# Kernel tuning notes

Hardware: AMD Instinct MI355X
Metric: run time of the kernel (lower is better)

## Reference

```python
import jax, jax.numpy as jnp
import numpy as np

N_NODES = 100000
N_EDGES = 3200000
D_IN = 128
D_OUT = 128
BN_EPS = 1e-5


def setup_inputs() -> dict:
    key = jax.random.key(0)
    k1, k2, k3, k4, k5 = jax.random.split(key, 5)
    x = jax.random.normal(k1, (N_NODES, D_IN), dtype=jnp.float32)
    edge_index = jax.random.randint(k2, (2, N_EDGES), 0, N_NODES, dtype=jnp.int64)
    s = 1.0 / np.sqrt(D_IN)
    W_l = jax.random.uniform(k3, (D_IN, D_OUT), minval=-s, maxval=s, dtype=jnp.float32)
    b_l = jnp.zeros((D_OUT,), dtype=jnp.float32)
    W_r = jax.random.uniform(k4, (D_IN, D_OUT), minval=-s, maxval=s, dtype=jnp.float32)
    gamma = jnp.ones((D_OUT,), dtype=jnp.float32)
    beta = jnp.zeros((D_OUT,), dtype=jnp.float32)
    return {"x": x, "edge_index": edge_index, "W_l": W_l, "b_l": b_l,
            "W_r": W_r, "gamma": gamma, "beta": beta}


def _sage_bn(x, edge_index, W_l, b_l, W_r, gamma, beta):
    src, dst = edge_index[0], edge_index[1]
    # gather source features, scatter-sum at targets, divide by in-degree (mean aggr)
    agg_sum = jax.ops.segment_sum(x[src], dst, num_segments=N_NODES)  # [N, D_IN]
    deg = jax.ops.segment_sum(jnp.ones((N_EDGES,), x.dtype), dst, num_segments=N_NODES)
    agg = agg_sum / jnp.maximum(deg, 1.0)[:, None]
    # SAGEConv: lin_l(aggregated) + lin_r(self)
    x_raw = agg @ W_l + b_l + x @ W_r  # [N, D_OUT]
    # BatchNorm1d (training mode: batch stats, biased variance)
    mu = jnp.mean(x_raw, axis=0)
    var = jnp.var(x_raw, axis=0)
    x_deskewed = (x_raw - mu) * jax.lax.rsqrt(var + BN_EPS) * gamma + beta
    return x_raw, x_deskewed


def reference(x, edge_index, W_l, b_l, W_r, gamma, beta):
    return _sage_bn(x, edge_index, W_l, b_l, W_r, gamma, beta)
```

## Files before the change

kernel.cpp:

```cpp
#include <hip/hip_runtime.h>

constexpr int NN = 100000;
constexpr int NE = 3200000;
constexpr int DD = 128;
constexpr int NB = 782;
constexpr int RND = 8192;
#define BN_EPS 1e-5f

typedef __attribute__((ext_vector_type(8))) short bf16x8;
typedef __attribute__((ext_vector_type(4))) float f32x4;
typedef __attribute__((ext_vector_type(2))) float f32x2;

constexpr size_t WS_CNT   = 0;
constexpr size_t WS_COFF  = 4096;
constexpr size_t WS_CUR   = 8192;
constexpr size_t WS_FLAG  = 12288;
constexpr size_t WS_BNSUM = 12800;
constexpr size_t WS_BNSQ  = 13312;
constexpr size_t WS_ZERO  = 16384;
constexpr size_t WS_DEG   = 16384;
constexpr size_t WS_OFF   = 416384;
constexpr size_t WS_CSR   = 816384;
constexpr size_t WS_WT    = 13616384;

__device__ inline unsigned bf16rne(float f) {
    unsigned u = __float_as_uint(f);
    return (u + 0x7fffu + ((u >> 16) & 1u)) >> 16;
}

#if __has_builtin(__builtin_amdgcn_cvt_pk_f32_fp8)
__device__ inline f32x2 fp8pk_lo(unsigned u) {
    return __builtin_amdgcn_cvt_pk_f32_fp8((int)u, false);
}
__device__ inline f32x2 fp8pk_hi(unsigned u) {
    return __builtin_amdgcn_cvt_pk_f32_fp8((int)u, true);
}
__device__ inline unsigned f32x4_to_fp8(float4 v) {
    int w = __builtin_amdgcn_cvt_pk_fp8_f32(v.x, v.y, 0, false);
    w = __builtin_amdgcn_cvt_pk_fp8_f32(v.z, v.w, w, true);
    return (unsigned)w;
}
#else
__device__ inline float fp8_to_f32_1(unsigned b) {
    unsigned s = (b & 0x80u) << 24;
    unsigned em = b & 0x7fu;
    float f;
    if (em >= 8) f = __uint_as_float((em << 20) + (120u << 23));
    else f = (float)em * 0.001953125f;
    return __uint_as_float(__float_as_uint(f) | s);
}
__device__ inline f32x2 fp8pk_lo(unsigned u) {
    f32x2 r;
    r[0] = fp8_to_f32_1(u & 0xffu);
    r[1] = fp8_to_f32_1((u >> 8) & 0xffu);
    return r;
}
__device__ inline f32x2 fp8pk_hi(unsigned u) {
    f32x2 r;
    r[0] = fp8_to_f32_1((u >> 16) & 0xffu);
    r[1] = fp8_to_f32_1((u >> 24) & 0xffu);
    return r;
}
__device__ inline unsigned f32_to_fp8_1(float f) {
    unsigned s = (__float_as_uint(f) >> 24) & 0x80u;
    float a = fabsf(f);
    if (!(a > 0.f)) return s;
    if (a >= 448.f) return s | 0x7Eu;
    int e = (int)(__float_as_uint(a) >> 23) - 127;
    if (e < -6) e = -6;
    float step = __uint_as_float((unsigned)(e - 3 + 127) << 23);
    int m = (int)rintf(a / step);
    if (m >= 16) { e += 1; m = 8; }
    if (m >= 8) return s | (unsigned)((e + 7) << 3) | (unsigned)(m - 8);
    return s | (unsigned)m;
}
__device__ inline unsigned f32x4_to_fp8(float4 v) {
    return f32_to_fp8_1(v.x) | (f32_to_fp8_1(v.y) << 8) |
           (f32_to_fp8_1(v.z) << 16) | (f32_to_fp8_1(v.w) << 24);
}
#endif

#define ACC8(u)                                                              \
    {                                                                        \
        aa0 += fp8pk_lo((u).x);                                              \
        aa1 += fp8pk_hi((u).x);                                              \
        aa2 += fp8pk_lo((u).y);                                              \
        aa3 += fp8pk_hi((u).y);                                              \
    }

__global__ void k_detect(const int* __restrict__ ei, int* __restrict__ flag) {
    int lane = threadIdx.x;
    int v = ei[2 * lane + 1];
    unsigned long long b = __ballot(v == 0);
    if (lane == 0) *flag = (b == ~0ull) ? 1 : 0;
}

__global__ __launch_bounds__(256) void k_prep(const float* __restrict__ x,
                                              unsigned* __restrict__ xb,
                                              unsigned* __restrict__ xq,
                                              const float* __restrict__ Wl,
                                              const float* __restrict__ Wr,
                                              unsigned short* __restrict__ Wt) {
    int bid = blockIdx.x;
    if (bid < 2048) {
        int total = NN * DD / 4;
        for (int i = bid * 256 + threadIdx.x; i < total; i += 2048 * 256) {
            float4 v = ((const float4*)x)[i];
            unsigned a = (bf16rne(v.y) << 16) | bf16rne(v.x);
            unsigned b = (bf16rne(v.w) << 16) | bf16rne(v.z);
            ((uint2*)xb)[i] = make_uint2(a, b);
            xq[i] = f32x4_to_fp8(v);
        }
    } else {
        int idx = (bid - 2048) * 256 + threadIdx.x;
        int n = idx >> 8, k = idx & 255;
        float v = (k < 128) ? Wl[(size_t)k * DD + n] : Wr[(size_t)(k - 128) * DD + n];
        Wt[idx] = (unsigned short)bf16rne(v);
    }
}

__global__ __launch_bounds__(256) void k_bcount(const int* __restrict__ ei,
                                                const int* __restrict__ flag,
                                                int* __restrict__ cnt) {
    __shared__ int hist[NB];
    for (int i = threadIdx.x; i < NB; i += 256) hist[i] = 0;
    __syncthreads();
    int i64 = *flag;
    int stride = gridDim.x * 256;
    for (int e = blockIdx.x * 256 + threadIdx.x; e < NE; e += stride) {
        int dst = i64 ? ei[2 * (NE + e)] : ei[NE + e];
        atomicAdd(&hist[dst >> 7], 1);
    }
    __syncthreads();
    for (int i = threadIdx.x; i < NB; i += 256) {
        int c = hist[i];
        if (c) atomicAdd(&cnt[i], c);
    }
}

__global__ __launch_bounds__(256) void k_scan(const int* __restrict__ cnt,
                                              int* __restrict__ coff,
                                              int* __restrict__ cur) {
    __shared__ int s[NB];
    for (int i = threadIdx.x; i < NB; i += 256) s[i] = cnt[i];
    __syncthreads();
    if (threadIdx.x == 0) {
        int acc = 0;
        for (int i = 0; i < NB; ++i) { int c = s[i]; s[i] = acc; acc += c; }
    }
    __syncthreads();
    for (int i = threadIdx.x; i < NB; i += 256) { coff[i] = s[i]; cur[i] = s[i]; }
    if (threadIdx.x == 0) coff[NB] = NE;
}

__global__ __launch_bounds__(256) void k_bin(const int* __restrict__ ei,
                                             const int* __restrict__ flag,
                                             int* __restrict__ cur,
                                             unsigned* __restrict__ bin) {
    __shared__ int hist[NB];
    __shared__ int sbs[NB];
    __shared__ int gbase[NB];
    __shared__ int rk[NB];
    __shared__ int wsum[256];
    __shared__ unsigned short sj[RND];
    int tid = threadIdx.x;
    for (int i = tid; i < NB; i += 256) { hist[i] = 0; rk[i] = 0; }
    __syncthreads();
    int i64 = *flag;
    int e0 = blockIdx.x * RND;
    int cntE = NE - e0; if (cntE > RND) cntE = RND;

    for (int j = tid; j < cntE; j += 256) {
        int e = e0 + j;
        int dst = i64 ? ei[2 * (NE + e)] : ei[NE + e];
        atomicAdd(&hist[dst >> 7], 1);
    }
    __syncthreads();

    int b4 = tid * 4;
    int l0 = (b4 + 0 < NB) ? hist[b4 + 0] : 0;
    int l1 = (b4 + 1 < NB) ? hist[b4 + 1] : 0;
    int l2 = (b4 + 2 < NB) ? hist[b4 + 2] : 0;
    int l3 = (b4 + 3 < NB) ? hist[b4 + 3] : 0;
    int tsum = l0 + l1 + l2 + l3;
    wsum[tid] = tsum;
    __syncthreads();
    for (int d = 1; d < 256; d <<= 1) {
        int v = (tid >= d) ? wsum[tid - d] : 0;
        __syncthreads();
        wsum[tid] += v;
        __syncthreads();
    }
    int p = wsum[tid] - tsum;
    if (b4 + 0 < NB) sbs[b4 + 0] = p;
    if (b4 + 1 < NB) sbs[b4 + 1] = p + l0;
    if (b4 + 2 < NB) sbs[b4 + 2] = p + l0 + l1;
    if (b4 + 3 < NB) sbs[b4 + 3] = p + l0 + l1 + l2;
    __syncthreads();

    for (int j = tid; j < cntE; j += 256) {
        int e = e0 + j;
        int dst = i64 ? ei[2 * (NE + e)] : ei[NE + e];
        int b = dst >> 7;
        int r = atomicAdd(&rk[b], 1);
        sj[sbs[b] + r] = (unsigned short)j;
    }
    for (int b = tid; b < NB; b += 256) {
        int c = hist[b];
        if (c > 0) gbase[b] = atomicAdd(&cur[b], c);
    }
    __syncthreads();

    for (int t = tid; t < cntE; t += 256) {
        int j = sj[t];
        int e = e0 + j;
        int src = i64 ? ei[2 * e] : ei[e];
        int dst = i64 ? ei[2 * (NE + e)] : ei[NE + e];
        int b = dst >> 7;
        bin[gbase[b] + (t - sbs[b])] = ((unsigned)src << 7) | (unsigned)(dst & 127);
    }
}

__global__ __launch_bounds__(256) void k_csr(const unsigned* __restrict__ bin,
                                             const int* __restrict__ coff,
                                             int* __restrict__ csr,
                                             int* __restrict__ deg,
                                             int* __restrict__ off) {
    __shared__ int hist[128];
    __shared__ int sb[128];
    __shared__ int curs[128];
    int b = blockIdx.x;
    int tid = threadIdx.x;
    if (tid < 128) hist[tid] = 0;
    __syncthreads();
    int e0 = coff[b], e1 = coff[b + 1];
    for (int j = e0 + tid; j < e1; j += 256)
        atomicAdd(&hist[bin[j] & 127], 1);
    __syncthreads();
    if (tid == 0) {
        int acc = 0;
        for (int i = 0; i < 128; ++i) { sb[i] = acc; acc += hist[i]; }
    }
    __syncthreads();
    if (tid < 128) curs[tid] = sb[tid];
    __syncthreads();
    for (int j = e0 + tid; j < e1; j += 256) {
        unsigned p = bin[j];
        int d = p & 127;
        int r = atomicAdd(&curs[d], 1);
        csr[e0 + r] = (int)(p >> 7);
    }
    int n = b * 128 + tid;
    if (tid < 128 && n < NN) {
        deg[n] = hist[tid];
        off[n] = e0 + sb[tid];
    }
}

__global__ __launch_bounds__(256) void k_agg(const uint2* __restrict__ xq2,
                                             const int* __restrict__ csr,
                                             const int* __restrict__ deg,
                                             const int* __restrict__ off,
                                             unsigned* __restrict__ aggb) {
    int w = (blockIdx.x * 256 + threadIdx.x) >> 6;
    int lane = threadIdx.x & 63;
    if (w >= NN) return;
    int dg = deg[w];
    int o = off[w];
    int q = lane >> 4;
    int cl = lane & 15;
    f32x2 aa0 = {0.f, 0.f}, aa1 = {0.f, 0.f}, aa2 = {0.f, 0.f}, aa3 = {0.f, 0.f};

    int j = 0;
    for (; j + 16 <= dg; j += 16) {
        int s0 = csr[o + j + q];
        int s1 = csr[o + j + 4 + q];
        int s2 = csr[o + j + 8 + q];
        int s3 = csr[o + j + 12 + q];
        uint2 u0 = xq2[(size_t)s0 * 16 + cl];
        uint2 u1 = xq2[(size_t)s1 * 16 + cl];
        uint2 u2 = xq2[(size_t)s2 * 16 + cl];
        uint2 u3 = xq2[(size_t)s3 * 16 + cl];
        ACC8(u0); ACC8(u1); ACC8(u2); ACC8(u3);
    }
    for (; j + 4 <= dg; j += 4) {
        int s = csr[o + j + q];
        uint2 u = xq2[(size_t)s * 16 + cl];
        ACC8(u);
    }
    int rem = dg - j;
    if (q < rem) {
        int s = csr[o + j + q];
        uint2 u = xq2[(size_t)s * 16 + cl];
        ACC8(u);
    }

    float a0 = aa0[0], a1 = aa0[1], a2 = aa1[0], a3 = aa1[1];
    float a4 = aa2[0], a5 = aa2[1], a6 = aa3[0], a7 = aa3[1];
    a0 += __shfl_xor(a0, 16); a0 += __shfl_xor(a0, 32);
    a1 += __shfl_xor(a1, 16); a1 += __shfl_xor(a1, 32);
    a2 += __shfl_xor(a2, 16); a2 += __shfl_xor(a2, 32);
    a3 += __shfl_xor(a3, 16); a3 += __shfl_xor(a3, 32);
    a4 += __shfl_xor(a4, 16); a4 += __shfl_xor(a4, 32);
    a5 += __shfl_xor(a5, 16); a5 += __shfl_xor(a5, 32);
    a6 += __shfl_xor(a6, 16); a6 += __shfl_xor(a6, 32);
    a7 += __shfl_xor(a7, 16); a7 += __shfl_xor(a7, 32);

    if (lane < 16) {
        float inv = 1.0f / fmaxf((float)dg, 1.0f);
        uint4 p;
        p.x = (bf16rne(a1 * inv) << 16) | bf16rne(a0 * inv);
        p.y = (bf16rne(a3 * inv) << 16) | bf16rne(a2 * inv);
        p.z = (bf16rne(a5 * inv) << 16) | bf16rne(a4 * inv);
        p.w = (bf16rne(a7 * inv) << 16) | bf16rne(a6 * inv);
        ((uint4*)aggb)[(size_t)w * 16 + cl] = p;
    }
}

__global__ __launch_bounds__(256) void k_gemm(const unsigned short* __restrict__ aggb,
                                              const unsigned short* __restrict__ xb,
                                              const unsigned short* __restrict__ Wt,
                                              const float* __restrict__ bl,
                                              float* __restrict__ out_raw,
                                              float* __restrict__ bn_sum,
                                              float* __restrict__ bn_sq) {
    __shared__ unsigned short sW[128][264];
    __shared__ float s_s[4][128];
    __shared__ float s_q[4][128];
    int tid = threadIdx.x;
    int wv = tid >> 6, lane = tid & 63;
    int l15 = lane & 15, lhi = lane >> 4;
    int mr = blockIdx.x * 128 + wv * 32;

    {
        const uint4* g = (const uint4*)Wt;
        #pragma unroll
        for (int it = 0; it < 16; ++it) {
            int c = tid + it * 256;
            int row = c >> 5;
            int col = (c & 31) * 8;
            *(uint4*)&sW[row][col] = g[c];
        }
    }

    int r0 = mr + l15;       if (r0 > NN - 1) r0 = NN - 1;
    int r1 = mr + 16 + l15;  if (r1 > NN - 1) r1 = NN - 1;
    const unsigned short* a0p = aggb + (size_t)r0 * DD;
    const unsigned short* a1p = aggb + (size_t)r1 * DD;
    const unsigned short* x0p = xb + (size_t)r0 * DD;
    const unsigned short* x1p = xb + (size_t)r1 * DD;

    f32x4 acc[2][8];
    #pragma unroll
    for (int m = 0; m < 2; ++m)
        #pragma unroll
        for (int nt = 0; nt < 8; ++nt)
            acc[m][nt] = (f32x4){0.f, 0.f, 0.f, 0.f};

    __syncthreads();

    #pragma unroll
    for (int ks = 0; ks < 8; ++ks) {
        int kk = (ks & 3) * 32 + lhi * 8;
        bf16x8 a0, a1;
        if (ks < 4) {
            a0 = *(const bf16x8*)(a0p + kk);
            a1 = *(const bf16x8*)(a1p + kk);
        } else {
            a0 = *(const bf16x8*)(x0p + kk);
            a1 = *(const bf16x8*)(x1p + kk);
        }
        #pragma unroll
        for (int nt = 0; nt < 8; ++nt) {
            bf16x8 b = *(const bf16x8*)&sW[nt * 16 + l15][ks * 32 + lhi * 8];
            acc[0][nt] = __builtin_amdgcn_mfma_f32_16x16x32_bf16(a0, b, acc[0][nt], 0, 0, 0);
            acc[1][nt] = __builtin_amdgcn_mfma_f32_16x16x32_bf16(a1, b, acc[1][nt], 0, 0, 0);
        }
    }

    float bias8[8];
    #pragma unroll
    for (int nt = 0; nt < 8; ++nt) bias8[nt] = bl[nt * 16 + l15];

    float s8[8] = {}, q8[8] = {};
    #pragma unroll
    for (int m = 0; m < 2; ++m) {
        #pragma unroll
        for (int r = 0; r < 4; ++r) {
            int row = mr + m * 16 + lhi * 4 + r;
            if (row < NN) {
                #pragma unroll
                for (int nt = 0; nt < 8; ++nt) {
                    float v = acc[m][nt][r] + bias8[nt];
                    out_raw[(size_t)row * DD + nt * 16 + l15] = v;
                    s8[nt] += v;
                    q8[nt] += v * v;
                }
            }
        }
    }

    #pragma unroll
    for (int nt = 0; nt < 8; ++nt) {
        s8[nt] += __shfl_xor(s8[nt], 16);
        s8[nt] += __shfl_xor(s8[nt], 32);
        q8[nt] += __shfl_xor(q8[nt], 16);
        q8[nt] += __shfl_xor(q8[nt], 32);
    }
    if (lhi == 0) {
        #pragma unroll
        for (int nt = 0; nt < 8; ++nt) {
            s_s[wv][nt * 16 + l15] = s8[nt];
            s_q[wv][nt * 16 + l15] = q8[nt];
        }
    }
    __syncthreads();
    if (tid < 128) {
        float ts = s_s[0][tid] + s_s[1][tid] + s_s[2][tid] + s_s[3][tid];
        float tq = s_q[0][tid] + s_q[1][tid] + s_q[2][tid] + s_q[3][tid];
        atomicAdd(&bn_sum[tid], ts);
        atomicAdd(&bn_sq[tid], tq);
    }
}

__global__ __launch_bounds__(256) void k_norm(const float* __restrict__ raw,
                                              const float* __restrict__ bn_sum,
                                              const float* __restrict__ bn_sq,
                                              const float* __restrict__ gamma,
                                              const float* __restrict__ beta,
                                              float* __restrict__ out) {
    const float invN = 1.0f / (float)NN;
    int total = NN * DD / 4;
    for (int idx = blockIdx.x * 256 + threadIdx.x; idx < total; idx += gridDim.x * 256) {
        int cp = idx & 31;
        float4 v = ((const float4*)raw)[idx];
        float4 s = ((const float4*)bn_sum)[cp];
        float4 q = ((const float4*)bn_sq)[cp];
        float4 g = ((const float4*)gamma)[cp];
        float4 b = ((const float4*)beta)[cp];
        float4 o;
        { float mu = s.x * invN; float var = q.x * invN - mu * mu;
          o.x = (v.x - mu) * rsqrtf(var + BN_EPS) * g.x + b.x; }
        { float mu = s.y * invN; float var = q.y * invN - mu * mu;
          o.y = (v.y - mu) * rsqrtf(var + BN_EPS) * g.y + b.y; }
        { float mu = s.z * invN; float var = q.z * invN - mu * mu;
          o.z = (v.z - mu) * rsqrtf(var + BN_EPS) * g.z + b.z; }
        { float mu = s.w * invN; float var = q.w * invN - mu * mu;
          o.w = (v.w - mu) * rsqrtf(var + BN_EPS) * g.w + b.w; }
        ((float4*)out)[idx] = o;
    }
}

extern "C" void kernel_launch(void* const* d_in, const int* in_sizes, int n_in,
                              void* d_out, int out_size, void* d_ws, size_t ws_size,
                              hipStream_t stream) {
    const float* x     = (const float*)d_in[0];
    const int*   ei    = (const int*)d_in[1];
    const float* Wl    = (const float*)d_in[2];
    const float* bl    = (const float*)d_in[3];
    const float* Wr    = (const float*)d_in[4];
    const float* gamma = (const float*)d_in[5];
    const float* beta  = (const float*)d_in[6];

    float* out_raw = (float*)d_out;
    float* out_bn  = out_raw + (size_t)NN * DD;
    unsigned* xq   = (unsigned*)d_out;
    unsigned* bin  = (unsigned*)out_bn;
    unsigned* aggb = (unsigned*)out_bn;
    unsigned* xb   = (unsigned*)((char*)out_bn + (size_t)NN * DD * 2);

    char* ws = (char*)d_ws;
    int*   cnt    = (int*)(ws + WS_CNT);
    int*   coff   = (int*)(ws + WS_COFF);
    int*   cur    = (int*)(ws + WS_CUR);
    int*   flag   = (int*)(ws + WS_FLAG);
    float* bn_sum = (float*)(ws + WS_BNSUM);
    float* bn_sq  = (float*)(ws + WS_BNSQ);
    int*   deg    = (int*)(ws + WS_DEG);
    int*   off    = (int*)(ws + WS_OFF);
    int*   csr    = (int*)(ws + WS_CSR);
    unsigned short* Wt = (unsigned short*)(ws + WS_WT);

    hipMemsetAsync(d_ws, 0, WS_ZERO, stream);

    k_detect<<<1, 64, 0, stream>>>(ei, flag);
    k_prep<<<2048 + 128, 256, 0, stream>>>(x, xb, xq, Wl, Wr, Wt);
    k_bcount<<<512, 256, 0, stream>>>(ei, flag, cnt);
    k_scan<<<1, 256, 0, stream>>>(cnt, coff, cur);
    k_bin<<<(NE + RND - 1) / RND, 256, 0, stream>>>(ei, flag, cur, bin);
    k_csr<<<NB, 256, 0, stream>>>(bin, coff, csr, deg, off);
    k_agg<<<(NN * 64 + 255) / 256, 256, 0, stream>>>((const uint2*)xq, csr, deg, off, aggb);
    k_gemm<<<(NN + 127) / 128, 256, 0, stream>>>((const unsigned short*)aggb,
                                                 (const unsigned short*)xb,
                                                 Wt, bl, out_raw, bn_sum, bn_sq);
    k_norm<<<4096, 256, 0, stream>>>(out_raw, bn_sum, bn_sq, gamma, beta, out_bn);
}
```

Before: 228.0 us.

## Vectorize edge histogram loads, prescale CSR indices, prefetch GEMM A operands

The bucket-count kernel now reads destination indices as int4 vectors, handling the int64 and int32 layouts separately, so it issues fewer and wider loads. CSR entries are stored pre-multiplied by 16, which drops the 64-bit multiply from the gather address in the aggregation kernel. The GEMM kernel loads all A fragments into registers before the MFMA loop so global loads overlap the weight staging. The register prefetch raises register pressure, and the scaled indices assume the node count times 16 fits in an int.

```diff
diff --git a/kernel.cpp b/kernel.cpp
--- a/kernel.cpp
+++ b/kernel.cpp
@@ -127,9 +127,24 @@
     __syncthreads();
     int i64 = *flag;
     int stride = gridDim.x * 256;
-    for (int e = blockIdx.x * 256 + threadIdx.x; e < NE; e += stride) {
-        int dst = i64 ? ei[2 * (NE + e)] : ei[NE + e];
-        atomicAdd(&hist[dst >> 7], 1);
+    if (i64) {
+        const int4* dp = (const int4*)(ei + 2 * (size_t)NE);
+        int total = NE / 2;
+        for (int i = blockIdx.x * 256 + threadIdx.x; i < total; i += stride) {
+            int4 v = dp[i];
+            atomicAdd(&hist[v.x >> 7], 1);
+            atomicAdd(&hist[v.z >> 7], 1);
+        }
+    } else {
+        const int4* dp = (const int4*)(ei + (size_t)NE);
+        int total = NE / 4;
+        for (int i = blockIdx.x * 256 + threadIdx.x; i < total; i += stride) {
+            int4 v = dp[i];
+            atomicAdd(&hist[v.x >> 7], 1);
+            atomicAdd(&hist[v.y >> 7], 1);
+            atomicAdd(&hist[v.z >> 7], 1);
+            atomicAdd(&hist[v.w >> 7], 1);
+        }
     }
     __syncthreads();
     for (int i = threadIdx.x; i < NB; i += 256) {
@@ -248,7 +263,7 @@
         unsigned p = bin[j];
         int d = p & 127;
         int r = atomicAdd(&curs[d], 1);
-        csr[e0 + r] = (int)(p >> 7);
+        csr[e0 + r] = (int)((p >> 7) << 4);
     }
     int n = b * 128 + tid;
     if (tid < 128 && n < NN) {
@@ -269,6 +284,7 @@
     int o = off[w];
     int q = lane >> 4;
     int cl = lane & 15;
+    const uint2* xp = xq2 + cl;
     f32x2 aa0 = {0.f, 0.f}, aa1 = {0.f, 0.f}, aa2 = {0.f, 0.f}, aa3 = {0.f, 0.f};
 
     int j = 0;
@@ -277,21 +293,21 @@
         int s1 = csr[o + j + 4 + q];
         int s2 = csr[o + j + 8 + q];
         int s3 = csr[o + j + 12 + q];
-        uint2 u0 = xq2[(size_t)s0 * 16 + cl];
-        uint2 u1 = xq2[(size_t)s1 * 16 + cl];
-        uint2 u2 = xq2[(size_t)s2 * 16 + cl];
-        uint2 u3 = xq2[(size_t)s3 * 16 + cl];
+        uint2 u0 = xp[s0];
+        uint2 u1 = xp[s1];
+        uint2 u2 = xp[s2];
+        uint2 u3 = xp[s3];
         ACC8(u0); ACC8(u1); ACC8(u2); ACC8(u3);
     }
     for (; j + 4 <= dg; j += 4) {
         int s = csr[o + j + q];
-        uint2 u = xq2[(size_t)s * 16 + cl];
+        uint2 u = xp[s];
         ACC8(u);
     }
     int rem = dg - j;
     if (q < rem) {
         int s = csr[o + j + q];
-        uint2 u = xq2[(size_t)s * 16 + cl];
+        uint2 u = xp[s];
         ACC8(u);
     }
 
@@ -350,6 +366,19 @@
     const unsigned short* x0p = xb + (size_t)r0 * DD;
     const unsigned short* x1p = xb + (size_t)r1 * DD;
 
+    bf16x8 A0[8], A1[8];
+    #pragma unroll
+    for (int ks = 0; ks < 8; ++ks) {
+        int kk = (ks & 3) * 32 + lhi * 8;
+        if (ks < 4) {
+            A0[ks] = *(const bf16x8*)(a0p + kk);
+            A1[ks] = *(const bf16x8*)(a1p + kk);
+        } else {
+            A0[ks] = *(const bf16x8*)(x0p + kk);
+            A1[ks] = *(const bf16x8*)(x1p + kk);
+        }
+    }
+
     f32x4 acc[2][8];
     #pragma unroll
     for (int m = 0; m < 2; ++m)
@@ -361,20 +390,11 @@
 
     #pragma unroll
     for (int ks = 0; ks < 8; ++ks) {
-        int kk = (ks & 3) * 32 + lhi * 8;
-        bf16x8 a0, a1;
-        if (ks < 4) {
-            a0 = *(const bf16x8*)(a0p + kk);
-            a1 = *(const bf16x8*)(a1p + kk);
-        } else {
-            a0 = *(const bf16x8*)(x0p + kk);
-            a1 = *(const bf16x8*)(x1p + kk);
-        }
         #pragma unroll
         for (int nt = 0; nt < 8; ++nt) {
             bf16x8 b = *(const bf16x8*)&sW[nt * 16 + l15][ks * 32 + lhi * 8];
-            acc[0][nt] = __builtin_amdgcn_mfma_f32_16x16x32_bf16(a0, b, acc[0][nt], 0, 0, 0);
-            acc[1][nt] = __builtin_amdgcn_mfma_f32_16x16x32_bf16(a1, b, acc[1][nt], 0, 0, 0);
+            acc[0][nt] = __builtin_amdgcn_mfma_f32_16x16x32_bf16(A0[ks], b, acc[0][nt], 0, 0, 0);
+            acc[1][nt] = __builtin_amdgcn_mfma_f32_16x16x32_bf16(A1[ks], b, acc[1][nt], 0, 0, 0);
         }
     }
 
```

Result: no change. 225.7 us (-1.0%).
